# Kernel optimization log

Measured on AMD Instinct MI355X. Metric: run time of the kernel, lower is better.

The kernel has to match this reference:

```python
import jax, jax.numpy as jnp
import numpy as np

ATTN, ENC, DEC = 1024, 1024, 1024
B, S = 64, 2048

def setup_inputs() -> dict:
    key = jax.random.key(0)
    k1, k2, k3, k4, k5, k6 = jax.random.split(key, 6)
    sc_w = 1.0 / np.sqrt(ENC + DEC)
    sc_v = 1.0 / np.sqrt(ATTN)
    return {
        "hidden": jax.random.normal(k1, (B, DEC), dtype=jnp.float32),
        "vectors_to_attend": jax.random.normal(k2, (S, B, ENC), dtype=jnp.float32),
        "attn_w_weight": jax.random.uniform(k3, (ATTN, ENC + DEC), jnp.float32, -sc_w, sc_w),
        "attn_w_bias": jax.random.uniform(k4, (ATTN,), jnp.float32, -sc_w, sc_w),
        "attn_v_weight": jax.random.uniform(k5, (1, ATTN), jnp.float32, -sc_v, sc_v),
        "attn_v_bias": jax.random.uniform(k6, (1,), jnp.float32, -sc_v, sc_v),
    }

def reference(hidden, vectors_to_attend, attn_w_weight, attn_w_bias, attn_v_weight, attn_v_bias):
    # vectors_to_attend: [S, B, E] -> [B, S, E]
    v = jnp.transpose(vectors_to_attend, (1, 0, 2))
    # Split attn_w over the concat dim: concat([v, h]) @ W^T == v @ We^T + h @ Wd^T
    We = attn_w_weight[:, :ENC]   # [A, E]
    Wd = attn_w_weight[:, ENC:]   # [A, D]
    # energies: [B, S, A]
    e = jnp.tanh(jnp.einsum('bse,ae->bsa', v, We)
                 + jnp.einsum('bd,ad->ba', hidden, Wd)[:, None, :]
                 + attn_w_bias)
    # scores: [B, S]
    scores = jnp.einsum('bsa,a->bs', e, attn_v_weight[0]) + attn_v_bias[0]
    weights = jax.nn.softmax(scores, axis=1)          # softmax over seq dim
    context = jnp.einsum('bs,bse->be', weights, v)    # [B, E]
    return context[:, None, :]                        # [B, 1, E] to match bmm output
```

## Files before the change

kernel.cpp:

```cpp
#include <hip/hip_runtime.h>
#include <hip/hip_bf16.h>
#include <math.h>

#define BB 64
#define SS 2048
#define MT (SS*BB)
#define NTL 32

typedef __attribute__((ext_vector_type(4))) float f4;
typedef __attribute__((ext_vector_type(8))) short s8;

__device__ __forceinline__ unsigned short f2bf(float x) {
  union { float f; unsigned u; } v; v.f = x;
  unsigned r = v.u + 0x7FFFu + ((v.u >> 16) & 1u);
  return (unsigned short)(r >> 16);
}
__device__ __forceinline__ float bf2f(unsigned short x) {
  union { unsigned u; float f; } v; v.u = ((unsigned)x) << 16;
  return v.f;
}
__device__ __forceinline__ float fast_tanh(float x) {
  float t = __expf(2.0f * x);
  return 1.0f - 2.0f * __builtin_amdgcn_rcpf(t + 1.0f);
}

#define GLD16(gp, lp) __builtin_amdgcn_global_load_lds( \
    (const __attribute__((address_space(1))) void*)(gp), \
    (__attribute__((address_space(3))) void*)(lp), 16, 0, 0)
#define WAITV4() asm volatile("s_waitcnt vmcnt(4)" ::: "memory")
#define WAITV0() asm volatile("s_waitcnt vmcnt(0)" ::: "memory")
#define BAR()    __builtin_amdgcn_s_barrier()

__global__ void k_pack(const float* __restrict__ src, unsigned short* __restrict__ dst,
                       int stride) {
  __shared__ float ls[64][260];
  int g = blockIdx.x, cb = blockIdx.y, tid = threadIdx.x;
  int cl = (tid & 63) * 4;
  int rb = tid >> 6;
  const float* s0 = src + (size_t)(g * 64) * stride + cb * 256 + cl;
  #pragma unroll
  for (int it = 0; it < 16; ++it) {
    int rr = it * 4 + rb;
    f4 x = *(const f4*)(s0 + (size_t)rr * stride);
    *(f4*)&ls[rr][cl] = x;
  }
  __syncthreads();
  int myKt = tid >> 5;
  int rr0 = (tid & 31) * 2;
  int panel = g >> 2;
  int prow0 = (g & 3) * 64 + rr0;
  #pragma unroll
  for (int rq = 0; rq < 2; ++rq) {
    int r = rr0 + rq, prow = prow0 + rq;
    int rsw = (prow >> 1) & 3;
    unsigned short* d = dst + (((size_t)panel * 32 + cb * 8 + myKt) * 256 + prow) * 32;
    #pragma unroll
    for (int s = 0; s < 4; ++s) {
      const float* sp = &ls[r][myKt * 32 + ((s ^ rsw) * 8)];
      f4 x0 = *(const f4*)sp, x1 = *(const f4*)(sp + 4);
      s8 o;
      #pragma unroll
      for (int j = 0; j < 4; ++j) { o[j] = (short)f2bf(x0[j]); o[4 + j] = (short)f2bf(x1[j]); }
      *(s8*)(d + s * 8) = o;
    }
  }
}

__global__ void k_hp(const float* __restrict__ hidden, const float* __restrict__ w,
                     const float* __restrict__ wbias, float* __restrict__ hp) {
  __shared__ float hs[1024];
  int b = blockIdx.x, tid = threadIdx.x;
  for (int i = tid; i < 1024; i += 256) hs[i] = hidden[b * 1024 + i];
  __syncthreads();
  int a = blockIdx.y * 256 + tid;
  const f4* wd = (const f4*)(w + a * 2048 + 1024);
  const f4* hv = (const f4*)hs;
  float acc = wbias[a];
  #pragma unroll 8
  for (int d = 0; d < 256; ++d) {
    f4 x = wd[d], y = hv[d];
    acc += x[0]*y[0] + x[1]*y[1] + x[2]*y[2] + x[3]*y[3];
  }
  hp[b * 1024 + a] = acc;
}

__global__ __launch_bounds__(512, 2) void k_gemm(
    const unsigned short* __restrict__ Avbs, const unsigned short* __restrict__ Wbs,
    const float* __restrict__ hp, const float* __restrict__ vw,
    float* __restrict__ part, int bm0, int nbm) {
  extern __shared__ char smem[];
  int bid = blockIdx.x;
  int nwg = nbm * 4;
  int wg = bid;
  if ((nwg & 7) == 0) { int cpx = nwg >> 3; wg = (bid & 7) * cpx + (bid >> 3); }
  int bn = wg & 3;
  int bmL = wg >> 2;
  int tid = threadIdx.x, lane = tid & 63;
  int wid = tid >> 6, wr = wid >> 2, wc = wid & 3;
  int c = lane & 15, kq = lane >> 4;

  int swz = kq ^ ((c >> 1) & 3);
  int a0 = (wr * 128 + c) * 64 + swz * 16;
  int b0 = (wc * 64 + c) * 64 + swz * 16;

  const unsigned short* Abase = Avbs + (size_t)bmL * 262144 + tid * 8;
  const unsigned short* Bbase = Wbs + (size_t)bn * 262144 + tid * 8;
  auto stageA = [&](int tt) {
    char* d = smem + (tt & 1) * 32768 + tid * 16;
    const unsigned short* s = Abase + (size_t)tt * 8192;
    GLD16(s, d); GLD16(s + 4096, d + 8192);
  };
  auto stageB = [&](int tt) {
    char* d = smem + (tt & 1) * 32768 + 16384 + tid * 16;
    const unsigned short* s = Bbase + (size_t)tt * 8192;
    GLD16(s, d); GLD16(s + 4096, d + 8192);
  };

  f4 acc[8][4];
  f4 z = {0.f, 0.f, 0.f, 0.f};
  #pragma unroll
  for (int i = 0; i < 8; ++i)
    #pragma unroll
    for (int j = 0; j < 4; ++j) acc[i][j] = z;

  stageA(0); stageB(0); stageA(1); stageB(1);
  WAITV4();
  BAR();

  s8 a[8];
  #pragma unroll 1
  for (int t = 0; t < NTL; ++t) {
    const char* ra = smem + (t & 1) * 32768;
    const char* rb = ra + 16384;
    #pragma unroll
    for (int mi = 0; mi < 8; ++mi) a[mi] = *(const s8*)(ra + a0 + mi * 1024);
    s8 bf0 = *(const s8*)(rb + b0);
    s8 bf1 = *(const s8*)(rb + b0 + 1024);
    BAR();
    if (t <= 29) stageA(t + 2);
    __builtin_amdgcn_s_setprio(1);
    #pragma unroll
    for (int mi = 0; mi < 8; ++mi) {
      acc[mi][0] = __builtin_amdgcn_mfma_f32_16x16x32_bf16(a[mi], bf0, acc[mi][0], 0, 0, 0);
      acc[mi][1] = __builtin_amdgcn_mfma_f32_16x16x32_bf16(a[mi], bf1, acc[mi][1], 0, 0, 0);
    }
    __builtin_amdgcn_s_setprio(0);
    BAR();
    s8 bf2 = *(const s8*)(rb + b0 + 2048);
    s8 bf3 = *(const s8*)(rb + b0 + 3072);
    BAR();
    if (t <= 29) stageB(t + 2);
    __builtin_amdgcn_s_setprio(1);
    #pragma unroll
    for (int mi = 0; mi < 8; ++mi) {
      acc[mi][2] = __builtin_amdgcn_mfma_f32_16x16x32_bf16(a[mi], bf2, acc[mi][2], 0, 0, 0);
      acc[mi][3] = __builtin_amdgcn_mfma_f32_16x16x32_bf16(a[mi], bf3, acc[mi][3], 0, 0, 0);
    }
    __builtin_amdgcn_s_setprio(0);
    if (t < 30) WAITV4();
    else if (t == 30) WAITV0();
    BAR();
  }

  int lg = kq;
  int bm = bm0 + bmL;
  float rs[8][4];
  #pragma unroll
  for (int mi = 0; mi < 8; ++mi)
    #pragma unroll
    for (int j = 0; j < 4; ++j) rs[mi][j] = 0.f;
  #pragma unroll
  for (int ni = 0; ni < 4; ++ni) {
    int a_col = bn * 256 + wc * 64 + ni * 16 + c;
    float vwa = vw[a_col];
    const float* hpa = hp + a_col;
    #pragma unroll
    for (int mi = 0; mi < 8; ++mi) {
      #pragma unroll
      for (int j = 0; j < 4; ++j) {
        int r = wr * 128 + mi * 16 + lg * 4 + j;
        int b = r & 63;
        float x = acc[mi][ni][j] + hpa[b * 1024];
        rs[mi][j] += fast_tanh(x) * vwa;
      }
    }
  }
  #pragma unroll
  for (int off = 1; off < 16; off <<= 1) {
    #pragma unroll
    for (int mi = 0; mi < 8; ++mi)
      #pragma unroll
      for (int j = 0; j < 4; ++j)
        rs[mi][j] += __shfl_xor(rs[mi][j], off, 64);
  }
  if (c == 0) {
    int p = bn * 4 + wc;
    #pragma unroll
    for (int mi = 0; mi < 8; ++mi)
      #pragma unroll
      for (int j = 0; j < 4; ++j) {
        int m = bm * 256 + wr * 128 + mi * 16 + lg * 4 + j;
        int b = m & 63, s = m >> 6;
        part[(size_t)p * MT + b * SS + s] = rs[mi][j];
      }
  }
}

__global__ void k_softmax(const float* __restrict__ part, float* __restrict__ wt) {
  int b = blockIdx.x, tid = threadIdx.x, lane = tid & 63, wid = tid >> 6;
  __shared__ float red[8];
  float sc[8];
  float mx = -1e30f;
  #pragma unroll
  for (int i = 0; i < 8; ++i) {
    int s = tid + i * 256;
    float a = 0.f;
    #pragma unroll
    for (int p = 0; p < 16; ++p) a += part[(size_t)p * MT + b * SS + s];
    sc[i] = a; mx = fmaxf(mx, a);
  }
  for (int o = 1; o < 64; o <<= 1) mx = fmaxf(mx, __shfl_xor(mx, o, 64));
  if (lane == 0) red[wid] = mx;
  __syncthreads();
  mx = fmaxf(fmaxf(red[0], red[1]), fmaxf(red[2], red[3]));
  float sum = 0.f;
  #pragma unroll
  for (int i = 0; i < 8; ++i) { sc[i] = expf(sc[i] - mx); sum += sc[i]; }
  for (int o = 1; o < 64; o <<= 1) sum += __shfl_xor(sum, o, 64);
  if (lane == 0) red[4 + wid] = sum;
  __syncthreads();
  sum = red[4] + red[5] + red[6] + red[7];
  float inv = 1.f / sum;
  #pragma unroll
  for (int i = 0; i < 8; ++i) wt[b * SS + tid + i * 256] = sc[i] * inv;
}

__global__ void k_ctx_bfs(const unsigned short* __restrict__ vbs, const float* __restrict__ wt,
                          float* __restrict__ ctxp) {
  int b = blockIdx.x, cch = blockIdx.y, tid = threadIdx.x;
  int e = tid * 4;
  int kt = e >> 5, qo = (e >> 3) & 3, off = e & 7;
  f4 acc = {0.f, 0.f, 0.f, 0.f};
  int s0 = cch * 128;
  const float* wrow = wt + b * SS;
  #pragma unroll 4
  for (int s = s0; s < s0 + 128; ++s) {
    float ws = wrow[s];
    int row = s * 64 + b;
    int bmW = row >> 8, r = row & 255;
    size_t addr = (((size_t)bmW * 32 + kt) * 256 + r) * 32 + ((qo ^ ((r >> 1) & 3)) << 3) + off;
    ushort4 u = *(const ushort4*)(vbs + addr);
    acc[0] += bf2f(u.x) * ws;
    acc[1] += bf2f(u.y) * ws;
    acc[2] += bf2f(u.z) * ws;
    acc[3] += bf2f(u.w) * ws;
  }
  *(f4*)(ctxp + (size_t)(cch * 64 + b) * 1024 + tid * 4) = acc;
}

__global__ void k_ctx_f32(const float* __restrict__ v, const float* __restrict__ wt,
                          float* __restrict__ ctxp) {
  int b = blockIdx.x, cch = blockIdx.y, tid = threadIdx.x;
  f4 acc = {0.f, 0.f, 0.f, 0.f};
  int s0 = cch * 128;
  const float* wrow = wt + b * SS;
  #pragma unroll 4
  for (int s = s0; s < s0 + 128; ++s) {
    float ws = wrow[s];
    const f4* vp = (const f4*)(v + (size_t)(s * 64 + b) * 1024);
    acc += vp[tid] * ws;
  }
  *(f4*)(ctxp + (size_t)(cch * 64 + b) * 1024 + tid * 4) = acc;
}

__global__ void k_out(const float* __restrict__ ctxp, float* __restrict__ out) {
  int b = blockIdx.x, tid = threadIdx.x;
  f4 acc = {0.f, 0.f, 0.f, 0.f};
  #pragma unroll
  for (int cch = 0; cch < 16; ++cch)
    acc += *(const f4*)(ctxp + (size_t)(cch * 64 + b) * 1024 + tid * 4);
  *(f4*)(out + b * 1024 + tid * 4) = acc;
}

extern "C" void kernel_launch(void* const* d_in, const int* in_sizes, int n_in,
                              void* d_out, int out_size, void* d_ws, size_t ws_size,
                              hipStream_t stream) {
  const float* hidden = (const float*)d_in[0];
  const float* v      = (const float*)d_in[1];
  const float* ww     = (const float*)d_in[2];
  const float* wbias  = (const float*)d_in[3];
  const float* vwgt   = (const float*)d_in[4];
  float* out = (float*)d_out;

  char* ws = (char*)d_ws;
  float*          hp   = (float*)(ws);
  unsigned short* wbs  = (unsigned short*)(ws + 262144);
  float*          part = (float*)(ws + 262144 + 2097152);
  float*          wt   = (float*)(ws + 262144 + 2097152 + 8388608);
  float*          ctxp = (float*)(ws + 262144 + 2097152 + 8388608 + 524288);
  size_t fixed = 262144 + 2097152 + 8388608 + 524288 + 4194304;
  unsigned short* vbs  = (unsigned short*)(ws + fixed);

  size_t avail = (ws_size > fixed) ? (ws_size - fixed) : 0;
  long rows_chunk = (long)(avail / 2048) & ~511L;
  if (rows_chunk > MT) rows_chunk = MT;
  if (rows_chunk < 512) rows_chunk = 512;
  int nchunks = (int)((MT + rows_chunk - 1) / rows_chunk);

  hipFuncSetAttribute((const void*)k_gemm, hipFuncAttributeMaxDynamicSharedMemorySize, 65536);

  k_pack<<<dim3(16, 4), 256, 0, stream>>>(ww, wbs, 2048);
  k_hp<<<dim3(64, 4), 256, 0, stream>>>(hidden, ww, wbias, hp);

  for (long r0 = 0; r0 < MT; r0 += rows_chunk) {
    long nr = MT - r0; if (nr > rows_chunk) nr = rows_chunk;
    int nbm = (int)(nr / 256);
    k_pack<<<dim3((int)(nr / 64), 4), 256, 0, stream>>>(v + (size_t)r0 * 1024, vbs, 1024);
    k_gemm<<<nbm * 4, 512, 65536, stream>>>(vbs, wbs, hp, vwgt, part, (int)(r0 / 256), nbm);
  }

  k_softmax<<<64, 256, 0, stream>>>(part, wt);
  if (nchunks == 1)
    k_ctx_bfs<<<dim3(64, 16), 256, 0, stream>>>(vbs, wt, ctxp);
  else
    k_ctx_f32<<<dim3(64, 16), 256, 0, stream>>>(v, wt, ctxp);
  k_out<<<64, 256, 0, stream>>>(ctxp, out);
}
```

Before: 590.7 us.

## Double K-tile depth in GEMM with new 64-wide packed layout and split staging

Repacks the bf16 panels to 64-element K tiles with an XOR swizzle over 8 slots, and splits each 256-row panel into two 128-row halves. The GEMM now runs 16 iterations of K=64 using 128KB of LDS double buffering, loading A in halves and staging four sub-tiles at staggered points to overlap loads with MFMA. This is meant to halve the number of loop iterations and barrier overheads per K. The cost is double the LDS per block, which likely drops occupancy from 2 blocks per CU to 1, and more barriers within each iteration.

```diff
diff --git a/kernel.cpp b/kernel.cpp
--- a/kernel.cpp
+++ b/kernel.cpp
@@ -5,7 +5,7 @@
 #define BB 64
 #define SS 2048
 #define MT (SS*BB)
-#define NTL 32
+#define NT 16
 
 typedef __attribute__((ext_vector_type(4))) float f4;
 typedef __attribute__((ext_vector_type(8))) short s8;
@@ -28,6 +28,7 @@
     (const __attribute__((address_space(1))) void*)(gp), \
     (__attribute__((address_space(3))) void*)(lp), 16, 0, 0)
 #define WAITV4() asm volatile("s_waitcnt vmcnt(4)" ::: "memory")
+#define WAITV2() asm volatile("s_waitcnt vmcnt(2)" ::: "memory")
 #define WAITV0() asm volatile("s_waitcnt vmcnt(0)" ::: "memory")
 #define BAR()    __builtin_amdgcn_s_barrier()
 
@@ -35,34 +36,29 @@
                        int stride) {
   __shared__ float ls[64][260];
   int g = blockIdx.x, cb = blockIdx.y, tid = threadIdx.x;
-  int cl = (tid & 63) * 4;
-  int rb = tid >> 6;
+  int cl = (tid & 63) * 4, rbk = tid >> 6;
   const float* s0 = src + (size_t)(g * 64) * stride + cb * 256 + cl;
   #pragma unroll
   for (int it = 0; it < 16; ++it) {
-    int rr = it * 4 + rb;
-    f4 x = *(const f4*)(s0 + (size_t)rr * stride);
-    *(f4*)&ls[rr][cl] = x;
+    int rr = it * 4 + rbk;
+    *(f4*)&ls[rr][cl] = *(const f4*)(s0 + (size_t)rr * stride);
   }
   __syncthreads();
-  int myKt = tid >> 5;
-  int rr0 = (tid & 31) * 2;
-  int panel = g >> 2;
-  int prow0 = (g & 3) * 64 + rr0;
-  #pragma unroll
-  for (int rq = 0; rq < 2; ++rq) {
-    int r = rr0 + rq, prow = prow0 + rq;
-    int rsw = (prow >> 1) & 3;
-    unsigned short* d = dst + (((size_t)panel * 32 + cb * 8 + myKt) * 256 + prow) * 32;
-    #pragma unroll
-    for (int s = 0; s < 4; ++s) {
-      const float* sp = &ls[r][myKt * 32 + ((s ^ rsw) * 8)];
-      f4 x0 = *(const f4*)sp, x1 = *(const f4*)(sp + 4);
-      s8 o;
-      #pragma unroll
-      for (int j = 0; j < 4; ++j) { o[j] = (short)f2bf(x0[j]); o[4 + j] = (short)f2bf(x1[j]); }
-      *(s8*)(d + s * 8) = o;
-    }
+  int kt_l = tid >> 6;
+  int rr = tid & 63;
+  int kt = cb * 4 + kt_l;
+  int grow = g * 64 + rr;
+  int panel = grow >> 8, pr = grow & 255, h = pr >> 7, r = pr & 127;
+  unsigned short* d = dst + (((size_t)panel * 16 + kt) * 2 + h) * 8192 + r * 64;
+  int rx = r & 7;
+  #pragma unroll
+  for (int sp = 0; sp < 8; ++sp) {
+    const float* q = &ls[rr][kt_l * 64 + ((sp ^ rx) * 8)];
+    f4 x0 = *(const f4*)q, x1 = *(const f4*)(q + 4);
+    s8 o;
+    #pragma unroll
+    for (int j = 0; j < 4; ++j) { o[j] = (short)f2bf(x0[j]); o[4 + j] = (short)f2bf(x1[j]); }
+    *(s8*)(d + sp * 8) = o;
   }
 }
 
@@ -99,21 +95,18 @@
   int wid = tid >> 6, wr = wid >> 2, wc = wid & 3;
   int c = lane & 15, kq = lane >> 4;
 
-  int swz = kq ^ ((c >> 1) & 3);
-  int a0 = (wr * 128 + c) * 64 + swz * 16;
-  int b0 = (wc * 64 + c) * 64 + swz * 16;
+  int sx0 = ((kq) ^ (c & 7)) << 4;
+  int sx1 = ((4 + kq) ^ (c & 7)) << 4;
+  int aoff = wr * 16384 + c * 128;
+  int boff = 32768 + (wc >> 1) * 16384 + ((wc & 1) * 64 + c) * 128;
 
   const unsigned short* Abase = Avbs + (size_t)bmL * 262144 + tid * 8;
   const unsigned short* Bbase = Wbs + (size_t)bn * 262144 + tid * 8;
-  auto stageA = [&](int tt) {
-    char* d = smem + (tt & 1) * 32768 + tid * 16;
-    const unsigned short* s = Abase + (size_t)tt * 8192;
-    GLD16(s, d); GLD16(s + 4096, d + 8192);
-  };
-  auto stageB = [&](int tt) {
-    char* d = smem + (tt & 1) * 32768 + 16384 + tid * 16;
-    const unsigned short* s = Bbase + (size_t)tt * 8192;
-    GLD16(s, d); GLD16(s + 4096, d + 8192);
+  auto stage = [&](int tt, int u) {
+    char* d = smem + (tt & 1) * 65536 + u * 16384 + tid * 16;
+    const unsigned short* s = ((u & 2) ? Bbase : Abase) + ((size_t)tt * 2 + (u & 1)) * 8192;
+    GLD16(s, d);
+    GLD16(s + 4096, d + 8192);
   };
 
   f4 acc[8][4];
@@ -123,44 +116,59 @@
     #pragma unroll
     for (int j = 0; j < 4; ++j) acc[i][j] = z;
 
-  stageA(0); stageB(0); stageA(1); stageB(1);
+  s8 va[4], vb0[4], vb1[4];
+
+#define LDA(rb, mh, SX) { const char* ba_ = (rb) + aoff + (mh) * 8192 + (SX); \
+    va[0] = *(const s8*)(ba_); va[1] = *(const s8*)(ba_ + 2048); \
+    va[2] = *(const s8*)(ba_ + 4096); va[3] = *(const s8*)(ba_ + 6144); }
+#define LDB(rb, VB, SX) { const char* bb_ = (rb) + boff + (SX); \
+    VB[0] = *(const s8*)(bb_); VB[1] = *(const s8*)(bb_ + 2048); \
+    VB[2] = *(const s8*)(bb_ + 4096); VB[3] = *(const s8*)(bb_ + 6144); }
+#define MM(mh, VB) { \
+    __builtin_amdgcn_s_setprio(1); \
+    _Pragma("unroll") \
+    for (int m_ = 0; m_ < 4; ++m_) { \
+      acc[(mh)*4+m_][0] = __builtin_amdgcn_mfma_f32_16x16x32_bf16(va[m_], VB[0], acc[(mh)*4+m_][0], 0, 0, 0); \
+      acc[(mh)*4+m_][1] = __builtin_amdgcn_mfma_f32_16x16x32_bf16(va[m_], VB[1], acc[(mh)*4+m_][1], 0, 0, 0); \
+      acc[(mh)*4+m_][2] = __builtin_amdgcn_mfma_f32_16x16x32_bf16(va[m_], VB[2], acc[(mh)*4+m_][2], 0, 0, 0); \
+      acc[(mh)*4+m_][3] = __builtin_amdgcn_mfma_f32_16x16x32_bf16(va[m_], VB[3], acc[(mh)*4+m_][3], 0, 0, 0); \
+    } \
+    __builtin_amdgcn_s_setprio(0); }
+
+  stage(0, 0); stage(0, 1); stage(0, 2); stage(0, 3);
+  stage(1, 2); stage(1, 3);
   WAITV4();
   BAR();
 
-  s8 a[8];
   #pragma unroll 1
-  for (int t = 0; t < NTL; ++t) {
-    const char* ra = smem + (t & 1) * 32768;
-    const char* rb = ra + 16384;
-    #pragma unroll
-    for (int mi = 0; mi < 8; ++mi) a[mi] = *(const s8*)(ra + a0 + mi * 1024);
-    s8 bf0 = *(const s8*)(rb + b0);
-    s8 bf1 = *(const s8*)(rb + b0 + 1024);
-    BAR();
-    if (t <= 29) stageA(t + 2);
-    __builtin_amdgcn_s_setprio(1);
-    #pragma unroll
-    for (int mi = 0; mi < 8; ++mi) {
-      acc[mi][0] = __builtin_amdgcn_mfma_f32_16x16x32_bf16(a[mi], bf0, acc[mi][0], 0, 0, 0);
-      acc[mi][1] = __builtin_amdgcn_mfma_f32_16x16x32_bf16(a[mi], bf1, acc[mi][1], 0, 0, 0);
-    }
-    __builtin_amdgcn_s_setprio(0);
-    BAR();
-    s8 bf2 = *(const s8*)(rb + b0 + 2048);
-    s8 bf3 = *(const s8*)(rb + b0 + 3072);
-    BAR();
-    if (t <= 29) stageB(t + 2);
-    __builtin_amdgcn_s_setprio(1);
-    #pragma unroll
-    for (int mi = 0; mi < 8; ++mi) {
-      acc[mi][2] = __builtin_amdgcn_mfma_f32_16x16x32_bf16(a[mi], bf2, acc[mi][2], 0, 0, 0);
-      acc[mi][3] = __builtin_amdgcn_mfma_f32_16x16x32_bf16(a[mi], bf3, acc[mi][3], 0, 0, 0);
-    }
-    __builtin_amdgcn_s_setprio(0);
-    if (t < 30) WAITV4();
-    else if (t == 30) WAITV0();
-    BAR();
-  }
+  for (int t = 0; t < NT; ++t) {
+    const char* rb = smem + (t & 1) * 65536;
+    LDA(rb, 0, sx0); LDB(rb, vb0, sx0);
+    if (t < 15) stage(t + 1, 0);
+    BAR();
+    MM(0, vb0);
+    BAR();
+    LDA(rb, 0, sx1); LDB(rb, vb1, sx1);
+    if (t < 15) stage(t + 1, 1);
+    BAR();
+    MM(0, vb1);
+    BAR();
+    LDA(rb, 1, sx0);
+    if (t < 14) stage(t + 2, 2);
+    BAR();
+    MM(1, vb0);
+    BAR();
+    LDA(rb, 1, sx1);
+    if (t < 14) stage(t + 2, 3);
+    BAR();
+    MM(1, vb1);
+    if (t < 14) WAITV2();
+    else if (t == 14) WAITV0();
+    BAR();
+  }
+#undef LDA
+#undef LDB
+#undef MM
 
   int lg = kq;
   int bm = bm0 + bmL;
@@ -239,7 +247,7 @@
                           float* __restrict__ ctxp) {
   int b = blockIdx.x, cch = blockIdx.y, tid = threadIdx.x;
   int e = tid * 4;
-  int kt = e >> 5, qo = (e >> 3) & 3, off = e & 7;
+  int kt = e >> 6, sl = (e >> 3) & 7, off = e & 7;
   f4 acc = {0.f, 0.f, 0.f, 0.f};
   int s0 = cch * 128;
   const float* wrow = wt + b * SS;
@@ -247,8 +255,8 @@
   for (int s = s0; s < s0 + 128; ++s) {
     float ws = wrow[s];
     int row = s * 64 + b;
-    int bmW = row >> 8, r = row & 255;
-    size_t addr = (((size_t)bmW * 32 + kt) * 256 + r) * 32 + ((qo ^ ((r >> 1) & 3)) << 3) + off;
+    int panel = row >> 8, pr = row & 255, h = pr >> 7, r = pr & 127;
+    size_t addr = (((size_t)panel * 16 + kt) * 2 + h) * 8192 + r * 64 + ((sl ^ (r & 7)) << 3) + off;
     ushort4 u = *(const ushort4*)(vbs + addr);
     acc[0] += bf2f(u.x) * ws;
     acc[1] += bf2f(u.y) * ws;
@@ -307,7 +315,7 @@
   if (rows_chunk < 512) rows_chunk = 512;
   int nchunks = (int)((MT + rows_chunk - 1) / rows_chunk);
 
-  hipFuncSetAttribute((const void*)k_gemm, hipFuncAttributeMaxDynamicSharedMemorySize, 65536);
+  hipFuncSetAttribute((const void*)k_gemm, hipFuncAttributeMaxDynamicSharedMemorySize, 131072);
 
   k_pack<<<dim3(16, 4), 256, 0, stream>>>(ww, wbs, 2048);
   k_hp<<<dim3(64, 4), 256, 0, stream>>>(hidden, ww, wbias, hp);
@@ -316,7 +324,7 @@
     long nr = MT - r0; if (nr > rows_chunk) nr = rows_chunk;
     int nbm = (int)(nr / 256);
     k_pack<<<dim3((int)(nr / 64), 4), 256, 0, stream>>>(v + (size_t)r0 * 1024, vbs, 1024);
-    k_gemm<<<nbm * 4, 512, 65536, stream>>>(vbs, wbs, hp, vwgt, part, (int)(r0 / 256), nbm);
+    k_gemm<<<nbm * 4, 512, 131072, stream>>>(vbs, wbs, hp, vwgt, part, (int)(r0 / 256), nbm);
   }
 
   k_softmax<<<64, 256, 0, stream>>>(part, wt);
```

Measured after the change: 586.6 us. Within noise of the previous version (-0.7%).
